# Performance work log

Hardware: AMD Instinct MI355X
Metric: run time of the kernel (lower is better)

The kernel has to match this reference:

```python
import jax, jax.numpy as jnp
import numpy as np

B, S, D, H, F, L = 16, 512, 512, 8, 2048, 3  # L layers: 1 in blocks_1 + 2 in blocks_2
DK = D // H
EPS = 1e-5

def setup_inputs():
    key = jax.random.key(0)
    ks = jax.random.split(key, 10)
    sc = 1.0 / np.sqrt(D)
    return dict(
        q_embed_data=jax.random.normal(ks[0], (B, S, D), jnp.float32),
        qa_embed_data=jax.random.normal(ks[1], (B, S, D), jnp.float32),
        Wk=jax.random.normal(ks[2], (L, D, D), jnp.float32) * sc,
        bk=jnp.zeros((L, D), jnp.float32),
        Wv=jax.random.normal(ks[3], (L, D, D), jnp.float32) * sc,
        bv=jnp.zeros((L, D), jnp.float32),
        Wo=jax.random.normal(ks[4], (L, D, D), jnp.float32) * sc,
        bo=jnp.zeros((L, D), jnp.float32),
        gammas=jax.random.normal(ks[5], (L, H, 1, 1), jnp.float32) * 0.5,
        ln1_g=jnp.ones((L, D), jnp.float32),
        ln1_b=jnp.zeros((L, D), jnp.float32),
        W1=jax.random.normal(ks[6], (L, D, F), jnp.float32) * sc,
        b1=jnp.zeros((L, F), jnp.float32),
        W2=jax.random.normal(ks[7], (L, F, D), jnp.float32) * (1.0 / np.sqrt(F)),
        b2=jnp.zeros((L, D), jnp.float32),
        ln2_g=jnp.ones((L, D), jnp.float32),
        ln2_b=jnp.zeros((L, D), jnp.float32),
    )

def _ln(x, g, b):
    m = jnp.mean(x, -1, keepdims=True)
    v = jnp.mean((x - m) ** 2, -1, keepdims=True)
    return (x - m) * jax.lax.rsqrt(v + EPS) * g + b

def _attention(q, k, v, mask, gamma):
    # q,k,v: [B,H,S,DK]; mask: [1,1,S,S] bool; gamma: [H,1,1]
    scores = jnp.einsum('bhid,bhjd->bhij', q, k) / np.sqrt(DK)
    maskf = mask.astype(scores.dtype)
    # first (no-grad in torch) softmax pass for distance decay
    p = jax.nn.softmax(jnp.where(mask, scores, -1e32), axis=-1) * maskf
    distcum = jnp.cumsum(p, axis=-1)
    disttot = jnp.sum(p, axis=-1, keepdims=True)
    idx = jnp.arange(scores.shape[-1])
    pos = jnp.abs(idx[None, :] - idx[:, None]).astype(scores.dtype)[None, None]
    dist = jax.lax.stop_gradient(
        jnp.sqrt(jnp.clip((disttot - distcum) * pos, 0.0, None)))
    g = -jax.nn.softplus(gamma)[None]  # [1,H,1,1]
    total_effect = jnp.clip(jnp.exp(dist * g), 1e-5, 1e5)
    scores = jnp.where(mask, scores * total_effect, -1e32)
    attn = jax.nn.softmax(scores, axis=-1)
    return jnp.einsum('bhij,bhjd->bhid', attn, v)

def _mha(q_in, k_in, v_in, mask, Wk, bk, Wv, bv, Wo, bo, gamma):
    bsz = q_in.shape[0]
    def proj(x, W, b):
        return (x @ W + b).reshape(bsz, -1, H, DK).transpose(0, 2, 1, 3)
    q = proj(q_in, Wk, bk)  # kq_same=True -> q uses k_linear
    k = proj(k_in, Wk, bk)
    v = proj(v_in, Wv, bv)
    o = _attention(q, k, v, mask, gamma)
    o = o.transpose(0, 2, 1, 3).reshape(bsz, -1, D)
    return o @ Wo + bo

def _block(i, mask, query, key, values, apply_pos, P):
    q2 = _mha(query, key, values, mask, P['Wk'][i], P['bk'][i], P['Wv'][i],
              P['bv'][i], P['Wo'][i], P['bo'][i], P['gammas'][i])
    x = _ln(query + q2, P['ln1_g'][i], P['ln1_b'][i])
    if apply_pos:
        h = jax.nn.relu(x @ P['W1'][i] + P['b1'][i]) @ P['W2'][i] + P['b2'][i]
        x = _ln(x + h, P['ln2_g'][i], P['ln2_b'][i])
    return x

def reference(q_embed_data, qa_embed_data, Wk, bk, Wv, bv, Wo, bo, gammas,
              ln1_g, ln1_b, W1, b1, W2, b2, ln2_g, ln2_b):
    P = dict(Wk=Wk, bk=bk, Wv=Wv, bv=bv, Wo=Wo, bo=bo, gammas=gammas,
             ln1_g=ln1_g, ln1_b=ln1_b, W1=W1, b1=b1, W2=W2, b2=b2,
             ln2_g=ln2_g, ln2_b=ln2_b)
    s = q_embed_data.shape[1]
    mask1 = jnp.tril(jnp.ones((s, s), bool))[None, None]        # mask==1: current+past
    mask0 = jnp.tril(jnp.ones((s, s), bool), -1)[None, None]    # mask==0: strictly past
    y = qa_embed_data
    x = q_embed_data
    y = _block(0, mask1, y, y, y, True, P)    # blocks_1: knowledge encoder
    x = _block(1, mask1, x, x, x, False, P)   # blocks_2: question encoder (no FFN)
    x = _block(2, mask0, x, x, y, True, P)    # blocks_2: knowledge retriever
    return x
```

## Files before the change

kernel.cpp:

```cpp
#include <hip/hip_runtime.h>
#include <hip/hip_bf16.h>

#define Bdim 16
#define Sdim 512
#define Ddim 512
#define Hdim 8
#define DKdim 64
#define Fdim 2048
#define Mrows (Bdim * Sdim)

typedef __attribute__((ext_vector_type(8))) short  frag16;
typedef __attribute__((ext_vector_type(4))) float  f32x4;
typedef __attribute__((ext_vector_type(8))) unsigned short ushort8;
typedef __attribute__((ext_vector_type(4))) unsigned short ushort4v;

#if defined(__has_builtin)
#  if __has_builtin(__builtin_amdgcn_exp2f)
#    define EXP2(x) __builtin_amdgcn_exp2f(x)
#  endif
#endif
#ifndef EXP2
#  define EXP2(x) __expf((x) * 0.6931471805599453f)
#endif
#define SC2 0.18033688011112042f

__device__ __forceinline__ unsigned short f2b(float x) {
    union { float f; unsigned int u; } v; v.f = x;
    unsigned int r = (v.u + 0x7FFFu + ((v.u >> 16) & 1u)) >> 16;
    return (unsigned short)r;
}

__global__ __launch_bounds__(256) void gemm_mfma(
    const __hip_bfloat16* __restrict__ A, const __hip_bfloat16* __restrict__ Bt,
    const float* __restrict__ bias, const float* __restrict__ R,
    float* __restrict__ Cf, unsigned short* __restrict__ Cb,
    int M, int N, int K, int do_relu)
{
    __shared__ short As[2][128 * 32];
    __shared__ short Bs[2][128 * 32];

    const int t = threadIdx.x;
    const int lane = t & 63;
    const int wave = t >> 6;

    const int gx = gridDim.x;
    const int nb = gx * gridDim.y;
    const int lid = blockIdx.x + gx * blockIdx.y;
    const int wid = (lid & 7) * (nb >> 3) + (lid >> 3);
    const int bm = (wid / gx) * 128;
    const int bn = (wid % gx) * 128;

    const int wm = (wave >> 1) * 64;
    const int wn = (wave & 1) * 64;

    f32x4 acc[4][4] = {};
    const int lrow = lane >> 2;
    const int lcol = (lane & 3) * 8;

    auto stage = [&](int k0, int buf) {
#pragma unroll
        for (int i = 0; i < 2; ++i) {
            const int chunk = wave * 2 + i;
            const int row = chunk * 16 + lrow;
            const __hip_bfloat16* ga = A + (size_t)(bm + row) * K + k0 + lcol;
            const __hip_bfloat16* gb = Bt + (size_t)(bn + row) * K + k0 + lcol;
            __builtin_amdgcn_global_load_lds(
                (const __attribute__((address_space(1))) unsigned int*)ga,
                (__attribute__((address_space(3))) unsigned int*)(&As[buf][chunk * 512]),
                16, 0, 0);
            __builtin_amdgcn_global_load_lds(
                (const __attribute__((address_space(1))) unsigned int*)gb,
                (__attribute__((address_space(3))) unsigned int*)(&Bs[buf][chunk * 512]),
                16, 0, 0);
        }
    };

    const int fr = lane & 15;
    const int quad = lane >> 4;
    const int nk = K >> 5;

    stage(0, 0);
    __syncthreads();

    for (int it = 0; it < nk; ++it) {
        const int buf = it & 1;
        if (it + 1 < nk) stage((it + 1) << 5, buf ^ 1);
        frag16 af[4], bfr[4];
#pragma unroll
        for (int i = 0; i < 4; ++i) {
            af[i]  = *(const frag16*)(&As[buf][(wm + i * 16 + fr) * 32 + quad * 8]);
            bfr[i] = *(const frag16*)(&Bs[buf][(wn + i * 16 + fr) * 32 + quad * 8]);
        }
#pragma unroll
        for (int mi = 0; mi < 4; ++mi)
#pragma unroll
            for (int ni = 0; ni < 4; ++ni)
                acc[mi][ni] = __builtin_amdgcn_mfma_f32_16x16x32_bf16(
                    af[mi], bfr[ni], acc[mi][ni], 0, 0, 0);
        __syncthreads();
    }

#pragma unroll
    for (int mi = 0; mi < 4; ++mi) {
#pragma unroll
        for (int r = 0; r < 4; ++r) {
            const int m = bm + wm + mi * 16 + quad * 4 + r;
#pragma unroll
            for (int ni = 0; ni < 4; ++ni) {
                const int n = bn + wn + ni * 16 + fr;
                float v = acc[mi][ni][r] + bias[n];
                if (R) v += R[(size_t)m * N + n];
                if (do_relu) v = fmaxf(v, 0.f);
                if (Cf) Cf[(size_t)m * N + n] = v;
                if (Cb) Cb[(size_t)m * N + n] = f2b(v);
            }
        }
    }
}

__global__ __launch_bounds__(256) void gemm_n64(
    const unsigned short* __restrict__ A0, const unsigned short* __restrict__ A1,
    const unsigned short* __restrict__ B0, const unsigned short* __restrict__ B1,
    const float* __restrict__ bias0, const float* __restrict__ bias1,
    const float* __restrict__ R, float* __restrict__ Cf,
    unsigned short* __restrict__ Cb, unsigned short* __restrict__ CbT,
    int K)
{
    const int NN = 512;
    __shared__ short As[2][128 * 32];
    __shared__ short Bs[2][64 * 32];

    const int trans = blockIdx.z;
    const unsigned short* A  = trans ? A1 : A0;
    const unsigned short* Bt = trans ? B1 : B0;
    const float* bias        = trans ? bias1 : bias0;

    const int t = threadIdx.x;
    const int lane = t & 63;
    const int wave = t >> 6;

    const int lid = blockIdx.x + 8 * blockIdx.y;
    const int wid = (lid & 7) * 64 + (lid >> 3);
    const int bm = (wid >> 3) * 128;
    const int bn = (wid & 7) * 64;

    const int wm = (wave >> 1) * 64;
    const int wn = (wave & 1) * 32;

    f32x4 acc[4][2] = {};
    const int lrow = lane >> 2;
    const int lcol = (lane & 3) * 8;

    auto stage = [&](int k0, int buf) {
#pragma unroll
        for (int i = 0; i < 2; ++i) {
            const int chunk = wave * 2 + i;
            const int row = chunk * 16 + lrow;
            const unsigned short* ga = A + (size_t)(bm + row) * K + k0 + lcol;
            __builtin_amdgcn_global_load_lds(
                (const __attribute__((address_space(1))) unsigned int*)ga,
                (__attribute__((address_space(3))) unsigned int*)(&As[buf][chunk * 512]),
                16, 0, 0);
        }
        {
            const int row = wave * 16 + lrow;
            const unsigned short* gb = Bt + (size_t)(bn + row) * K + k0 + lcol;
            __builtin_amdgcn_global_load_lds(
                (const __attribute__((address_space(1))) unsigned int*)gb,
                (__attribute__((address_space(3))) unsigned int*)(&Bs[buf][wave * 512]),
                16, 0, 0);
        }
    };

    const int fr = lane & 15;
    const int quad = lane >> 4;
    const int nk = K >> 5;

    stage(0, 0);
    __syncthreads();

    for (int it = 0; it < nk; ++it) {
        const int buf = it & 1;
        if (it + 1 < nk) stage((it + 1) << 5, buf ^ 1);
        frag16 af[4], bfr[2];
#pragma unroll
        for (int i = 0; i < 4; ++i)
            af[i] = *(const frag16*)(&As[buf][(wm + i * 16 + fr) * 32 + quad * 8]);
#pragma unroll
        for (int i = 0; i < 2; ++i)
            bfr[i] = *(const frag16*)(&Bs[buf][(wn + i * 16 + fr) * 32 + quad * 8]);
#pragma unroll
        for (int mi = 0; mi < 4; ++mi)
#pragma unroll
            for (int ni = 0; ni < 2; ++ni)
                acc[mi][ni] = __builtin_amdgcn_mfma_f32_16x16x32_bf16(
                    af[mi], bfr[ni], acc[mi][ni], 0, 0, 0);
        __syncthreads();
    }

    if (trans) {
#pragma unroll
        for (int mi = 0; mi < 4; ++mi)
#pragma unroll
            for (int ni = 0; ni < 2; ++ni) {
                const int m = bm + wm + mi * 16 + quad * 4;
                const int n = bn + wn + ni * 16 + fr;
                ushort4v o;
#pragma unroll
                for (int r = 0; r < 4; ++r) o[r] = f2b(acc[mi][ni][r] + bias[n]);
                const int bb = m >> 9, s = m & 511;
                const int hh = n >> 6, dd = n & 63;
                *(ushort4v*)(CbT + (((size_t)((bb * Hdim + hh) * DKdim + dd)) << 9) + s) = o;
            }
        return;
    }

#pragma unroll
    for (int mi = 0; mi < 4; ++mi) {
#pragma unroll
        for (int r = 0; r < 4; ++r) {
            const int m = bm + wm + mi * 16 + quad * 4 + r;
#pragma unroll
            for (int ni = 0; ni < 2; ++ni) {
                const int n = bn + wn + ni * 16 + fr;
                float v = acc[mi][ni][r] + bias[n];
                if (R) v += R[(size_t)m * NN + n];
                if (Cf) Cf[(size_t)m * NN + n] = v;
                if (Cb) Cb[(size_t)m * NN + n] = f2b(v);
            }
        }
    }
}

__global__ __launch_bounds__(256) void conv_b(
    const float* __restrict__ X, unsigned short* __restrict__ Y)
{
    const size_t i = ((size_t)blockIdx.x * 256 + threadIdx.x) * 8;
    float4 a = *(const float4*)(X + i);
    float4 b = *(const float4*)(X + i + 4);
    ushort8 o;
    o[0] = f2b(a.x); o[1] = f2b(a.y); o[2] = f2b(a.z); o[3] = f2b(a.w);
    o[4] = f2b(b.x); o[5] = f2b(b.y); o[6] = f2b(b.z); o[7] = f2b(b.w);
    *(ushort8*)(Y + i) = o;
}

__global__ __launch_bounds__(256) void wtrans_all(
    const float* __restrict__ Wk, const float* __restrict__ Wv,
    const float* __restrict__ Wo, const float* __restrict__ W1,
    const float* __restrict__ W2, unsigned short* __restrict__ dst)
{
    const int bid = blockIdx.x;
    const float* src; unsigned short* d; int K, N, tk, tn;
    if (bid < 576) {
        const int mat = bid >> 6, tile = bid & 63;
        const int l = mat / 3, wch = mat % 3;
        const float* W = (wch == 0) ? Wk : (wch == 1) ? Wv : Wo;
        src = W + (size_t)l * 262144;
        d = dst + (size_t)mat * 262144;
        K = 512; N = 512; tn = tile & 7; tk = tile >> 3;
    } else if (bid < 1088) {
        const int idx = bid - 576, l2 = idx >> 8, tile = idx & 255;
        src = W1 + (size_t)(l2 * 2) * (512 * 2048);
        d = dst + 9 * 262144 + (size_t)l2 * (512 * 2048);
        K = 512; N = 2048; tn = tile & 31; tk = tile >> 5;
    } else {
        const int idx = bid - 1088, l2 = idx >> 8, tile = idx & 255;
        src = W2 + (size_t)(l2 * 2) * (2048 * 512);
        d = dst + 9 * 262144 + 2 * (512 * 2048) + (size_t)l2 * (2048 * 512);
        K = 2048; N = 512; tn = tile & 7; tk = tile >> 3;
    }
    const int n0 = tn * 64, k0 = tk * 64;
    __shared__ float T[64][65];
    const int t = threadIdx.x;
    const int kl = t >> 4, n4 = (t & 15) << 2;
#pragma unroll
    for (int it = 0; it < 4; ++it) {
        const int k = kl + it * 16;
        float4 v = *(const float4*)(src + (size_t)(k0 + k) * N + n0 + n4);
        T[n4 + 0][k] = v.x; T[n4 + 1][k] = v.y;
        T[n4 + 2][k] = v.z; T[n4 + 3][k] = v.w;
    }
    __syncthreads();
    const int nl = t >> 3, k8 = (t & 7) << 3;
#pragma unroll
    for (int it = 0; it < 2; ++it) {
        const int n = nl + it * 32;
        ushort8 o;
#pragma unroll
        for (int c = 0; c < 8; ++c) o[c] = f2b(T[n][k8 + c]);
        *(ushort8*)(d + (size_t)(n0 + n) * K + k0 + k8) = o;
    }
}

__global__ __launch_bounds__(256, 8) void attn_flash8(
    const unsigned short* __restrict__ Kb,
    const unsigned short* __restrict__ Vt,
    const float* __restrict__ gam,
    unsigned short* __restrict__ Ob,
    int mask_type)
{
    __shared__ float CTw[16 * 33];
    __shared__ unsigned short Pst[4][16 * 36];
    __shared__ float S1s[4][16];
    __shared__ float S2s[4][16];
    __shared__ float OaccA[16 * 66];
    __shared__ float OaccB[16 * 66];

    const int h = blockIdx.x & 7, b = blockIdx.x >> 3;
    const int rk = blockIdx.y;
    const int tile = mask_type ? (31 - rk) : (rk == 0 ? 0 : 32 - rk);

    const int t = threadIdx.x, lane = t & 63, w = t >> 6;
    const int quad = lane >> 4, fr = lane & 15;
    const int q0 = tile * 16;
    const int iRow = q0 + fr;

    const unsigned short* kbase = Kb + (size_t)b * Sdim * Ddim + h * DKdim;
    const unsigned short* vtb = Vt + (size_t)(b * Hdim + h) * DKdim * Sdim;
    const float gneg2 = -log1pf(__expf(gam[h])) * 1.4426950408889634f;

    frag16 aq0 = *(const frag16*)(kbase + (size_t)(q0 + fr) * Ddim + quad * 8);
    frag16 aq1 = *(const frag16*)(kbase + (size_t)(q0 + fr) * Ddim + 32 + quad * 8);

    float psum = 0.f;
    for (int jn = w; jn <= tile; jn += 4) {
        frag16 k0 = *(const frag16*)(kbase + (size_t)(jn * 16 + fr) * Ddim + quad * 8);
        frag16 k1 = *(const frag16*)(kbase + (size_t)(jn * 16 + fr) * Ddim + 32 + quad * 8);
        f32x4 z = {0.f, 0.f, 0.f, 0.f};
        z = __builtin_amdgcn_mfma_f32_16x16x32_bf16(k0, aq0, z, 0, 0, 0);
        z = __builtin_amdgcn_mfma_f32_16x16x32_bf16(k1, aq1, z, 0, 0, 0);
        float tq = 0.f;
        if (jn < tile) {
#pragma unroll
            for (int r = 0; r < 4; ++r) tq += EXP2(z[r] * SC2);
        } else {
#pragma unroll
            for (int r = 0; r < 4; ++r) {
                const bool valid = mask_type ? (quad * 4 + r <= fr)
                                             : (quad * 4 + r < fr);
                tq += valid ? EXP2(z[r] * SC2) : 0.f;
            }
        }
        psum += tq;
        float tt = tq;
        tt += __shfl_xor(tt, 16);
        tt += __shfl_xor(tt, 32);
        if (quad == 0) CTw[fr * 33 + jn] = tt;
    }
    {
        float s1 = psum;
        s1 += __shfl_xor(s1, 16);
        s1 += __shfl_xor(s1, 32);
        if (lane < 16) S1s[w][lane] = s1;
    }
    __syncthreads();

    if (w == 0 && lane < 16) {
        float run = 0.f;
        for (int jn = tile; jn >= 0; --jn) {
            const float tv = CTw[lane * 33 + jn];
            CTw[lane * 33 + jn] = run;
            run += tv;
        }
    }
    __syncthreads();

    const float rsum1 = 1.f / (S1s[0][fr] + S1s[1][fr] + S1s[2][fr] + S1s[3][fr]);
    unsigned short* Pw = Pst[w];
    const bool fm_blk = (mask_type == 0) && (tile == 0);
    const bool fmrow = fm_blk && (fr == 0);
    const int umax = fm_blk ? (Sdim / 32 - 1) : (tile >> 1);
    float sum2p = 0.f;
    f32x4 oacc[4] = {};

    for (int u = umax - w; u >= 0; u -= 4) {
#pragma unroll
        for (int half = 0; half < 2; ++half) {
            const int jn = 2 * u + half;
            uint2 pku;
            if (jn > tile) {
                const unsigned int pv = fmrow ? 0x3F803F80u : 0u;
                pku.x = pv; pku.y = pv;
                sum2p += fmrow ? 4.f : 0.f;
            } else {
                frag16 k0 = *(const frag16*)(kbase + (size_t)(jn * 16 + fr) * Ddim + quad * 8);
                frag16 k1 = *(const frag16*)(kbase + (size_t)(jn * 16 + fr) * Ddim + 32 + quad * 8);
                f32x4 z = {0.f, 0.f, 0.f, 0.f};
                z = __builtin_amdgcn_mfma_f32_16x16x32_bf16(k0, aq0, z, 0, 0, 0);
                z = __builtin_amdgcn_mfma_f32_16x16x32_bf16(k1, aq1, z, 0, 0, 0);
                const bool full = (jn < tile);
                float s2r[4], lsuf[4];
                float tq = 0.f;
#pragma unroll
                for (int r = 3; r >= 0; --r) {
                    lsuf[r] = tq;
                    s2r[r] = z[r] * SC2;
                    float e1 = EXP2(s2r[r]);
                    if (!full) {
                        const bool valid = mask_type ? (quad * 4 + r <= fr)
                                                     : (quad * 4 + r < fr);
                        e1 = valid ? e1 : 0.f;
                    }
                    tq += e1;
                }
                float incl = tq;
                {
                    float u1 = __shfl_down(incl, 16);
                    incl += (quad < 3) ? u1 : 0.f;
                    float u2 = __shfl_down(incl, 32);
                    incl += (quad < 2) ? u2 : 0.f;
                }
                const float base = CTw[fr * 33 + jn] + (incl - tq);
                const float pos0 = (float)(iRow - (jn * 16 + quad * 4));
                float e2v[4];
#pragma unroll
                for (int r = 0; r < 4; ++r) {
                    const float ratio = (base + lsuf[r]) * rsum1;
                    const float arg = ratio * fabsf(pos0 - (float)r);
                    const float te = fmaxf(EXP2(gneg2 * sqrtf(arg)), 1e-5f);
                    float e2 = EXP2(s2r[r] * te);
                    if (!full) {
                        const bool valid = mask_type ? (quad * 4 + r <= fr)
                                                     : (quad * 4 + r < fr);
                        e2 = valid ? e2 : (fmrow ? 1.f : 0.f);
                    }
                    sum2p += e2;
                    e2v[r] = e2;
                }
                union { __hip_bfloat162 hh; unsigned int u; } c0, c1;
                c0.hh = __float22bfloat162_rn(make_float2(e2v[0], e2v[1]));
                c1.hh = __float22bfloat162_rn(make_float2(e2v[2], e2v[3]));
                pku.x = c0.u; pku.y = c1.u;
            }
            *(uint2*)(Pw + fr * 36 + half * 16 + quad * 4) = pku;
        }
        frag16 pf = *(const frag16*)(Pw + fr * 36 + quad * 8);
        const int jb = u * 32;
#pragma unroll
        for (int dt = 0; dt < 4; ++dt) {
            frag16 vf = *(const frag16*)(vtb + (size_t)(dt * 16 + fr) * Sdim + jb + quad * 8);
            oacc[dt] = __builtin_amdgcn_mfma_f32_16x16x32_bf16(pf, vf, oacc[dt], 0, 0, 0);
        }
    }

    {
        float s2 = sum2p;
        s2 += __shfl_xor(s2, 16);
        s2 += __shfl_xor(s2, 32);
        if (lane < 16) S2s[w][lane] = s2;
    }
    if (w == 1) {
#pragma unroll
        for (int dt = 0; dt < 4; ++dt)
#pragma unroll
            for (int r = 0; r < 4; ++r)
                OaccA[(quad * 4 + r) * 66 + dt * 16 + fr] = oacc[dt][r];
    }
    if (w == 3) {
#pragma unroll
        for (int dt = 0; dt < 4; ++dt)
#pragma unroll
            for (int r = 0; r < 4; ++r)
                OaccB[(quad * 4 + r) * 66 + dt * 16 + fr] = oacc[dt][r];
    }
    __syncthreads();
    if (w == 0) {
#pragma unroll
        for (int dt = 0; dt < 4; ++dt)
#pragma unroll
            for (int r = 0; r < 4; ++r)
                oacc[dt][r] += OaccA[(quad * 4 + r) * 66 + dt * 16 + fr];
    }
    if (w == 2) {
#pragma unroll
        for (int dt = 0; dt < 4; ++dt)
#pragma unroll
            for (int r = 0; r < 4; ++r)
                oacc[dt][r] += OaccB[(quad * 4 + r) * 66 + dt * 16 + fr];
    }
    __syncthreads();
    if (w == 2) {
#pragma unroll
        for (int dt = 0; dt < 4; ++dt)
#pragma unroll
            for (int r = 0; r < 4; ++r)
                OaccA[(quad * 4 + r) * 66 + dt * 16 + fr] = oacc[dt][r];
    }
    __syncthreads();

    if (w == 0) {
        const float rs2 = 1.f / (S2s[0][fr] + S2s[1][fr] + S2s[2][fr] + S2s[3][fr]);
        float rs2q[4];
#pragma unroll
        for (int r = 0; r < 4; ++r) rs2q[r] = __shfl(rs2, quad * 4 + r);

        unsigned short* obase = Ob + ((size_t)(b * Sdim + q0)) * Ddim + h * DKdim;
#pragma unroll
        for (int dt = 0; dt < 4; ++dt)
#pragma unroll
            for (int r = 0; r < 4; ++r) {
                const float v = oacc[dt][r] + OaccA[(quad * 4 + r) * 66 + dt * 16 + fr];
                obase[(size_t)(quad * 4 + r) * Ddim + dt * 16 + fr] = f2b(v * rs2q[r]);
            }
    }
}

__global__ __launch_bounds__(256) void ln_kernel(
    const float* __restrict__ X, const float* __restrict__ g,
    const float* __restrict__ bta, float* __restrict__ Y,
    unsigned short* __restrict__ Yb)
{
    const int row = blockIdx.x;
    const int t = threadIdx.x;
    __shared__ float r1[256], r2[256];
    const float* x = X + (size_t)row * Ddim;
    float a = x[t], b = x[t + 256];
    r1[t] = a + b;
    r2[t] = a * a + b * b;
    __syncthreads();
    for (int off = 128; off; off >>= 1) {
        if (t < off) { r1[t] += r1[t + off]; r2[t] += r2[t + off]; }
        __syncthreads();
    }
    float mean = r1[0] * (1.f / Ddim);
    float var = r2[0] * (1.f / Ddim) - mean * mean;
    float rs = rsqrtf(var + 1e-5f);
    float y0 = (a - mean) * rs * g[t] + bta[t];
    float y1 = (b - mean) * rs * g[t + 256] + bta[t + 256];
    if (Y) {
        float* y = Y + (size_t)row * Ddim;
        y[t] = y0;
        y[t + 256] = y1;
    }
    if (Yb) {
        unsigned short* yb = Yb + (size_t)row * Ddim;
        yb[t] = f2b(y0);
        yb[t + 256] = f2b(y1);
    }
}

extern "C" void kernel_launch(void* const* d_in, const int* in_sizes, int n_in,
                              void* d_out, int out_size, void* d_ws, size_t ws_size,
                              hipStream_t stream)
{
    const float* x0     = (const float*)d_in[0];
    const float* y0     = (const float*)d_in[1];
    const float* Wk     = (const float*)d_in[2];
    const float* bk     = (const float*)d_in[3];
    const float* Wv     = (const float*)d_in[4];
    const float* bv     = (const float*)d_in[5];
    const float* Wo     = (const float*)d_in[6];
    const float* bo     = (const float*)d_in[7];
    const float* gammas = (const float*)d_in[8];
    const float* ln1g   = (const float*)d_in[9];
    const float* ln1b   = (const float*)d_in[10];
    const float* W1     = (const float*)d_in[11];
    const float* b1     = (const float*)d_in[12];
    const float* W2     = (const float*)d_in[13];
    const float* b2     = (const float*)d_in[14];
    const float* ln2g   = (const float*)d_in[15];
    const float* ln2b   = (const float*)d_in[16];

    const size_t NBSD = (size_t)Mrows * Ddim;
    float* ws = (float*)d_ws;
    float* T1   = ws;
    float* X1   = T1 + NBSD;
    float* Xbuf = X1 + NBSD;
    unsigned short* Kbf = (unsigned short*)(Xbuf + NBSD);
    unsigned short* Vt  = Kbf + NBSD;
    unsigned short* AOb = Vt + NBSD;
    unsigned short* Abf = AOb + NBSD;
    unsigned short* Xbf = Abf + NBSD;
    unsigned short* Ybf = Xbf + NBSD;
    unsigned short* Hbb = Ybf + NBSD;
    unsigned short* WtAll = Hbb + (size_t)Mrows * Fdim;

    auto WtK = [&](int l) { return WtAll + (size_t)(l * 3 + 0) * 262144; };
    auto WtV = [&](int l) { return WtAll + (size_t)(l * 3 + 1) * 262144; };
    auto WtO = [&](int l) { return WtAll + (size_t)(l * 3 + 2) * 262144; };
    auto Wt1 = [&](int l) { return WtAll + 9 * 262144 + (size_t)(l >> 1) * (512 * 2048); };
    auto Wt2 = [&](int l) { return WtAll + 9 * 262144 + 2 * (512 * 2048) + (size_t)(l >> 1) * (2048 * 512); };

    const int convBlocks = (int)(NBSD / 2048);

    wtrans_all<<<1600, 256, 0, stream>>>(Wk, Wv, Wo, W1, W2, WtAll);

    auto run_block = [&](int l, const float* qinf, const unsigned short* qinb,
                         const unsigned short* vinb, int mask_type, bool ffn,
                         float* outf, unsigned short* outb) {
        const float* bk_l = bk + (size_t)l * Ddim;
        const float* bv_l = bv + (size_t)l * Ddim;
        const float* bo_l = bo + (size_t)l * Ddim;

        gemm_n64<<<dim3(8, 64, 2), 256, 0, stream>>>(
            qinb, vinb, WtK(l), WtV(l), bk_l, bv_l,
            nullptr, nullptr, Kbf, Vt, Ddim);
        attn_flash8<<<dim3(Bdim * Hdim, Sdim / 16, 1), 256, 0, stream>>>(
            Kbf, Vt, gammas + (size_t)l * Hdim, AOb, mask_type);
        gemm_n64<<<dim3(8, 64, 1), 256, 0, stream>>>(
            AOb, AOb, WtO(l), WtO(l), bo_l, bo_l,
            qinf, T1, nullptr, nullptr, Ddim);
        float* x1f = ffn ? X1 : outf;
        unsigned short* x1b = ffn ? Abf : outb;
        ln_kernel<<<Mrows, 256, 0, stream>>>(T1,
            ln1g + (size_t)l * Ddim, ln1b + (size_t)l * Ddim, x1f, x1b);
        if (ffn) {
            const float* b1_l = b1 + (size_t)l * Fdim;
            const float* b2_l = b2 + (size_t)l * Ddim;
            gemm_mfma<<<dim3(Fdim / 128, Mrows / 128), 256, 0, stream>>>(
                (const __hip_bfloat16*)Abf, (const __hip_bfloat16*)Wt1(l),
                b1_l, nullptr, nullptr, Hbb, Mrows, Fdim, Ddim, 1);
            gemm_n64<<<dim3(8, 64, 1), 256, 0, stream>>>(
                Hbb, Hbb, Wt2(l), Wt2(l), b2_l, b2_l,
                X1, T1, nullptr, nullptr, Fdim);
            ln_kernel<<<Mrows, 256, 0, stream>>>(T1,
                ln2g + (size_t)l * Ddim, ln2b + (size_t)l * Ddim, outf, outb);
        }
    };

    conv_b<<<convBlocks, 256, 0, stream>>>(y0, Abf);
    run_block(0, y0, Abf, Abf, 1, true, nullptr, Ybf);
    conv_b<<<convBlocks, 256, 0, stream>>>(x0, Abf);
    run_block(1, x0, Abf, Abf, 1, false, Xbuf, Xbf);
    run_block(2, Xbuf, Xbf, Ybf, 0, true, (float*)d_out, nullptr);
}
```

Baseline: 627.7 us.

## Double K-tile depth to 64 with XOR-swizzled LDS layout in gemm_n64

The N=64 GEMM now stages 64-wide K slices per iteration instead of 32, halving the number of barrier-separated loop iterations. The LDS layout is XOR-swizzled on 16-byte slots, with the swizzle applied to the global source address so that direct-to-LDS loads and fragment reads avoid bank conflicts. This doubles shared memory per block, which may reduce occupancy. Fragment registers also double because two K sub-steps are loaded before the MFMAs issue.

```diff
diff --git a/kernel.cpp b/kernel.cpp
--- a/kernel.cpp
+++ b/kernel.cpp
@@ -127,8 +127,8 @@
     int K)
 {
     const int NN = 512;
-    __shared__ short As[2][128 * 32];
-    __shared__ short Bs[2][64 * 32];
+    __shared__ short As[2][128 * 64];
+    __shared__ short Bs[2][64 * 64];
 
     const int trans = blockIdx.z;
     const unsigned short* A  = trans ? A1 : A0;
@@ -148,53 +148,61 @@
     const int wn = (wave & 1) * 32;
 
     f32x4 acc[4][2] = {};
-    const int lrow = lane >> 2;
-    const int lcol = (lane & 3) * 8;
+
+    const int srcslot = (((lane & 7) ^ (lane >> 3)) << 3);
+    const int rsub = lane >> 3;
 
     auto stage = [&](int k0, int buf) {
 #pragma unroll
-        for (int i = 0; i < 2; ++i) {
-            const int chunk = wave * 2 + i;
-            const int row = chunk * 16 + lrow;
-            const unsigned short* ga = A + (size_t)(bm + row) * K + k0 + lcol;
+        for (int i = 0; i < 4; ++i) {
+            const int row = i * 32 + wave * 8 + rsub;
+            const unsigned short* ga = A + (size_t)(bm + row) * K + k0 + srcslot;
             __builtin_amdgcn_global_load_lds(
                 (const __attribute__((address_space(1))) unsigned int*)ga,
-                (__attribute__((address_space(3))) unsigned int*)(&As[buf][chunk * 512]),
+                (__attribute__((address_space(3))) unsigned int*)(&As[buf][(i * 256 + wave * 64) * 8]),
                 16, 0, 0);
         }
-        {
-            const int row = wave * 16 + lrow;
-            const unsigned short* gb = Bt + (size_t)(bn + row) * K + k0 + lcol;
+#pragma unroll
+        for (int i = 0; i < 2; ++i) {
+            const int row = i * 32 + wave * 8 + rsub;
+            const unsigned short* gb = Bt + (size_t)(bn + row) * K + k0 + srcslot;
             __builtin_amdgcn_global_load_lds(
                 (const __attribute__((address_space(1))) unsigned int*)gb,
-                (__attribute__((address_space(3))) unsigned int*)(&Bs[buf][wave * 512]),
+                (__attribute__((address_space(3))) unsigned int*)(&Bs[buf][(i * 256 + wave * 64) * 8]),
                 16, 0, 0);
         }
     };
 
     const int fr = lane & 15;
     const int quad = lane >> 4;
-    const int nk = K >> 5;
+    const int sw = (fr & 7) << 3;
+    const int nk = K >> 6;
 
     stage(0, 0);
     __syncthreads();
 
     for (int it = 0; it < nk; ++it) {
         const int buf = it & 1;
-        if (it + 1 < nk) stage((it + 1) << 5, buf ^ 1);
-        frag16 af[4], bfr[2];
-#pragma unroll
-        for (int i = 0; i < 4; ++i)
-            af[i] = *(const frag16*)(&As[buf][(wm + i * 16 + fr) * 32 + quad * 8]);
-#pragma unroll
-        for (int i = 0; i < 2; ++i)
-            bfr[i] = *(const frag16*)(&Bs[buf][(wn + i * 16 + fr) * 32 + quad * 8]);
-#pragma unroll
-        for (int mi = 0; mi < 4; ++mi)
-#pragma unroll
-            for (int ni = 0; ni < 2; ++ni)
-                acc[mi][ni] = __builtin_amdgcn_mfma_f32_16x16x32_bf16(
-                    af[mi], bfr[ni], acc[mi][ni], 0, 0, 0);
+        if (it + 1 < nk) stage((it + 1) << 6, buf ^ 1);
+        frag16 af[2][4], bfr[2][2];
+#pragma unroll
+        for (int ks = 0; ks < 2; ++ks) {
+            const int col = (ks * 32 + quad * 8) ^ sw;
+#pragma unroll
+            for (int i = 0; i < 4; ++i)
+                af[ks][i] = *(const frag16*)(&As[buf][(wm + i * 16 + fr) * 64 + col]);
+#pragma unroll
+            for (int i = 0; i < 2; ++i)
+                bfr[ks][i] = *(const frag16*)(&Bs[buf][(wn + i * 16 + fr) * 64 + col]);
+        }
+#pragma unroll
+        for (int ks = 0; ks < 2; ++ks)
+#pragma unroll
+            for (int mi = 0; mi < 4; ++mi)
+#pragma unroll
+                for (int ni = 0; ni < 2; ++ni)
+                    acc[mi][ni] = __builtin_amdgcn_mfma_f32_16x16x32_bf16(
+                        af[ks][mi], bfr[ks][ni], acc[mi][ni], 0, 0, 0);
         __syncthreads();
     }
 
```

Result: faster. 611.7 us (-2.5%).
